# Kernel optimization log

Hardware: AMD Instinct MI355X
Metric: run time of the kernel (lower is better)

Reference implementation:

```python
import jax, jax.numpy as jnp
import numpy as np

FUTURE_K = 16
NEG_BIG = -1e9  # matches masked softmax semantics (invalid slots get exactly 0 weight in fp32)


def setup_inputs() -> dict:
    key = jax.random.key(0)
    hidden_states = jax.random.normal(key, (2, 4096, 1024), dtype=jnp.float32)
    return {"hidden_states": hidden_states}


def reference(hidden_states) -> jnp.ndarray:
    # Windowed future attention: for each position t, attend over the next
    # FUTURE_K hidden states (t+1 .. t+k), masked at the sequence end.
    B, S, H = hidden_states.shape
    k = FUTURE_K
    # pad on the right so every window is full-length
    x_padded = jnp.pad(hidden_states, ((0, 0), (0, k), (0, 0)))  # (B, S+k, H)
    t = jnp.arange(S)
    gidx = t[:, None] + 1 + jnp.arange(k)[None, :]               # (S, k) global indices
    windows = x_padded[:, gidx]                                   # (B, S, k, H)
    valid = gidx < S                                              # (S, k)
    # per-window dot-product scores, masked softmax over window slots
    scores = jnp.einsum('bth,btjh->btj', hidden_states, windows)  # (B, S, k)
    scores = jnp.where(valid[None], scores, NEG_BIG)
    weights = jax.nn.softmax(scores, axis=-1)
    # rows with no valid future (last positions) -> zero summary (torch nan_to_num)
    weights = jnp.where(valid[None], weights, 0.0)
    summary = jnp.einsum('btj,btjh->bth', weights, windows)       # (B, S, H)
    return summary
```

## Files before the change

### kernel.cpp

```cpp
#include <hip/hip_runtime.h>


typedef float f32x4 __attribute__((ext_vector_type(4)));
typedef unsigned int u32;
typedef u32 u32x4 __attribute__((ext_vector_type(4)));
typedef short bf16x8 __attribute__((ext_vector_type(8)));

namespace {
constexpr int kB = 2, kS = 4096, kH = 1024;
constexpr int kWaves = 8;
constexpr int kTilesT = 16;
constexpr int kBlocks = kB * kS / kTilesT;
constexpr int kXCD = 8;
constexpr int kHW = kH / kWaves;
}

__device__ __forceinline__ u32 f32u(float x){ return __builtin_bit_cast(u32, x); }
__device__ __forceinline__ float uf32(u32 x){ return __builtin_bit_cast(float, x); }
__device__ __forceinline__ u32 pkbf(float a, float b){ return (f32u(b)&0xFFFF0000u)|(f32u(a)>>16); }

struct Frag2 { bf16x8 hi, lo; };
__device__ __forceinline__ Frag2 split2(float4 u, float4 v) {
  float fu[8] = {u.x,u.y,u.z,u.w,v.x,v.y,v.z,v.w};
  u32 hw[4], lw[4];
#pragma unroll
  for (int i = 0; i < 4; ++i) {
    float a = fu[2*i], b = fu[2*i+1];
    u32 ua = f32u(a), ub = f32u(b);
    hw[i] = (ub & 0xFFFF0000u) | (ua >> 16);
    float la = a - uf32(ua & 0xFFFF0000u);
    float lb = b - uf32(ub & 0xFFFF0000u);
    lw[i] = (f32u(lb) & 0xFFFF0000u) | (f32u(la) >> 16);
  }
  Frag2 r;
  u32x4 h = {hw[0],hw[1],hw[2],hw[3]}, l = {lw[0],lw[1],lw[2],lw[3]};
  r.hi = __builtin_bit_cast(bf16x8, h);
  r.lo = __builtin_bit_cast(bf16x8, l);
  return r;
}

#define MFMA(A,B,C) __builtin_amdgcn_mfma_f32_16x16x32_bf16((A),(B),(C),0,0,0)

__global__ __launch_bounds__(512, 4)
void fenc_mfma(const float* __restrict__ x, float* __restrict__ out) {
  __shared__ float red[kWaves][2][4][64];
  const int lane = (int)(threadIdx.x & 63), wid = (int)(threadIdx.x >> 6);
  const int g = lane >> 4, c = lane & 15;

  const int vb  = (int)(blockIdx.x % kXCD)*(kBlocks/kXCD) + (int)(blockIdx.x / kXCD);
  const int t0g = vb * kTilesT;
  const int b   = t0g / kS, t0 = t0g % kS;
  const float* __restrict__ xb = x + (size_t)b*kS*kH;
  float* __restrict__ ob = out + (size_t)b*kS*kH;
  const int hw0 = kHW * wid;

  const int ra = (t0 + 1 + c  < kS) ? (t0 + 1 + c)  : (kS - 1);
  const int rb = (t0 + 17 + c < kS) ? (t0 + 17 + c) : (kS - 1);
  const float* qp  = xb + (size_t)(t0 + c)*kH + hw0;
  const float* kpa = xb + (size_t)ra*kH + hw0;
  const float* kpb = xb + (size_t)rb*kH + hw0;

  f32x4 aHH = {0.f,0.f,0.f,0.f}, aHL = aHH, aLH = aHH;
  f32x4 bHH = aHH, bHL = aHH, bLH = aHH;
  __builtin_amdgcn_s_setprio(1);
#pragma unroll
  for (int ks = 0; ks < 4; ++ks) {
    const int off = ks*32 + g*8;
    float4 q0 = *(const float4*)(qp  + off), q1 = *(const float4*)(qp  + off + 4);
    float4 a0 = *(const float4*)(kpa + off), a1 = *(const float4*)(kpa + off + 4);
    float4 b0 = *(const float4*)(kpb + off), b1 = *(const float4*)(kpb + off + 4);
    Frag2 fq = split2(q0, q1), fa = split2(a0, a1), fb = split2(b0, b1);
    aHH = MFMA(fa.hi, fq.hi, aHH);
    aHL = MFMA(fa.hi, fq.lo, aHL);
    aLH = MFMA(fa.lo, fq.hi, aLH);
    bHH = MFMA(fb.hi, fq.hi, bHH);
    bHL = MFMA(fb.hi, fq.lo, bHL);
    bLH = MFMA(fb.lo, fq.hi, bLH);
  }
  __builtin_amdgcn_s_setprio(0);
  f32x4 accA = (aHH + aHL) + aLH;
  f32x4 accB = (bHH + bHL) + bLH;

  const float* vrow[8];
#pragma unroll
  for (int i = 0; i < 8; ++i) {
    const int rv = t0 + 1 + 8*g + i;
    vrow[i] = xb + (size_t)((rv < kS) ? rv : (kS - 1))*kH + hw0 + c;
  }
  float vf[8][8];
#pragma unroll
  for (int nt = 0; nt < 8; ++nt)
#pragma unroll
    for (int i = 0; i < 8; ++i) vf[nt][i] = vrow[i][16*nt];

#pragma unroll
  for (int r = 0; r < 4; ++r) {
    red[wid][0][r][lane] = accA[r];
    red[wid][1][r][lane] = accB[r];
  }
  __syncthreads();
#pragma unroll
  for (int w = 0; w < kWaves; ++w) {
    if (w != wid) {
#pragma unroll
      for (int r = 0; r < 4; ++r) {
        accA[r] += red[w][0][r][lane];
        accB[r] += red[w][1][r][lane];
      }
    }
  }

  float p[2][4];
  float vmax = -1e30f;
#pragma unroll
  for (int T = 0; T < 2; ++T)
#pragma unroll
    for (int r = 0; r < 4; ++r) {
      const int w = 16*T + 4*g + r;
      const bool val = (w >= c) && (w < c + 16) && (t0 + 1 + w < kS);
      const float sv = val ? (T ? accB[r] : accA[r]) : -1e30f;
      p[T][r] = sv;
      vmax = fmaxf(vmax, sv);
    }
  vmax = fmaxf(vmax, __shfl_xor(vmax, 16, 64));
  vmax = fmaxf(vmax, __shfl_xor(vmax, 32, 64));
  float psum = 0.f;
#pragma unroll
  for (int T = 0; T < 2; ++T)
#pragma unroll
    for (int r = 0; r < 4; ++r) {
      const int w = 16*T + 4*g + r;
      const bool val = (w >= c) && (w < c + 16) && (t0 + 1 + w < kS);
      const float e = val ? __expf(p[T][r] - vmax) : 0.f;
      p[T][r] = e;
      psum += e;
    }
  psum += __shfl_xor(psum, 16, 64);
  psum += __shfl_xor(psum, 32, 64);
  const float inv = (psum > 0.f) ? (1.f / psum) : 0.f;
#pragma unroll
  for (int T = 0; T < 2; ++T)
#pragma unroll
    for (int r = 0; r < 4; ++r) p[T][r] *= inv;

  const int se = (g & 1)*32 + c, so = se + 16;
  float slot[8];
#pragma unroll
  for (int r = 0; r < 4; ++r) {
    const float e0 = __shfl(p[0][r], se, 64), e1 = __shfl(p[1][r], se, 64);
    const float o0 = __shfl(p[0][r], so, 64), o1 = __shfl(p[1][r], so, 64);
    slot[r]     = (g >> 1) ? e1 : e0;
    slot[4 + r] = (g >> 1) ? o1 : o0;
  }
  u32x4 pw = { pkbf(slot[0],slot[1]), pkbf(slot[2],slot[3]),
               pkbf(slot[4],slot[5]), pkbf(slot[6],slot[7]) };
  const bf16x8 pa = __builtin_bit_cast(bf16x8, pw);

  f32x4 o[8];
  __builtin_amdgcn_s_setprio(1);
#pragma unroll
  for (int nt = 0; nt < 8; ++nt) {
    u32x4 vw = { pkbf(vf[nt][0],vf[nt][1]), pkbf(vf[nt][2],vf[nt][3]),
                 pkbf(vf[nt][4],vf[nt][5]), pkbf(vf[nt][6],vf[nt][7]) };
    const bf16x8 vfrag = __builtin_bit_cast(bf16x8, vw);
    f32x4 z = {0.f,0.f,0.f,0.f};
    o[nt] = MFMA(pa, vfrag, z);
  }
  __builtin_amdgcn_s_setprio(0);

  float* orow[4];
#pragma unroll
  for (int r = 0; r < 4; ++r)
    orow[r] = ob + (size_t)(t0 + 4*g + r)*kH + hw0 + c;
#pragma unroll
  for (int nt = 0; nt < 8; ++nt)
#pragma unroll
    for (int r = 0; r < 4; ++r)
      orow[r][16*nt] = o[nt][r];
}

extern "C" void kernel_launch(void* const* d_in, const int* in_sizes, int n_in,
                              void* d_out, int out_size, void* d_ws, size_t ws_size,
                              hipStream_t stream) {
  const float* x = (const float*)d_in[0];
  float* out = (float*)d_out;
  hipLaunchKernelGGL(fenc_mfma, dim3(kBlocks), dim3(512), 0, stream, x, out);
}
```

Before: 25.41 us.

## Split hidden dimension of PV output across two blocks per tile

After: 48.81 us. 92.1% more time.

```diff
diff --git a/kernel.cpp b/kernel.cpp
--- a/kernel.cpp
+++ b/kernel.cpp
@@ -10,9 +10,11 @@
 constexpr int kB = 2, kS = 4096, kH = 1024;
 constexpr int kWaves = 8;
 constexpr int kTilesT = 16;
-constexpr int kBlocks = kB * kS / kTilesT;
+constexpr int kHSplit = 2;
+constexpr int kBlocks = kHSplit * kB * kS / kTilesT;
 constexpr int kXCD = 8;
-constexpr int kHW = kH / kWaves;
+constexpr int kHW  = kH / kWaves;
+constexpr int kHPV = kH / kHSplit / kWaves;
 }
 
 __device__ __forceinline__ u32 f32u(float x){ return __builtin_bit_cast(u32, x); }
@@ -41,18 +43,20 @@
 
 #define MFMA(A,B,C) __builtin_amdgcn_mfma_f32_16x16x32_bf16((A),(B),(C),0,0,0)
 
-__global__ __launch_bounds__(512, 4)
+__global__ __launch_bounds__(512, 8)
 void fenc_mfma(const float* __restrict__ x, float* __restrict__ out) {
-  __shared__ float red[kWaves][2][4][64];
+  __shared__ f32x4 red[kWaves][2][64];
   const int lane = (int)(threadIdx.x & 63), wid = (int)(threadIdx.x >> 6);
   const int g = lane >> 4, c = lane & 15;
 
   const int vb  = (int)(blockIdx.x % kXCD)*(kBlocks/kXCD) + (int)(blockIdx.x / kXCD);
-  const int t0g = vb * kTilesT;
+  const int tile = vb >> 1, q = vb & 1;
+  const int t0g = tile * kTilesT;
   const int b   = t0g / kS, t0 = t0g % kS;
   const float* __restrict__ xb = x + (size_t)b*kS*kH;
   float* __restrict__ ob = out + (size_t)b*kS*kH;
-  const int hw0 = kHW * wid;
+  const int hw0  = kHW * wid;
+  const int hpv0 = q * (kH / kHSplit) + kHPV * wid;
 
   const int ra = (t0 + 1 + c  < kS) ? (t0 + 1 + c)  : (kS - 1);
   const int rb = (t0 + 17 + c < kS) ? (t0 + 17 + c) : (kS - 1);
@@ -85,28 +89,19 @@
 #pragma unroll
   for (int i = 0; i < 8; ++i) {
     const int rv = t0 + 1 + 8*g + i;
-    vrow[i] = xb + (size_t)((rv < kS) ? rv : (kS - 1))*kH + hw0 + c;
+    vrow[i] = xb + (size_t)((rv < kS) ? rv : (kS - 1))*kH + hpv0 + c;
   }
-  float vf[8][8];
-#pragma unroll
-  for (int nt = 0; nt < 8; ++nt)
-#pragma unroll
-    for (int i = 0; i < 8; ++i) vf[nt][i] = vrow[i][16*nt];
 
-#pragma unroll
-  for (int r = 0; r < 4; ++r) {
-    red[wid][0][r][lane] = accA[r];
-    red[wid][1][r][lane] = accB[r];
-  }
+  red[wid][0][lane] = accA;
+  red[wid][1][lane] = accB;
   __syncthreads();
 #pragma unroll
   for (int w = 0; w < kWaves; ++w) {
     if (w != wid) {
-#pragma unroll
-      for (int r = 0; r < 4; ++r) {
-        accA[r] += red[w][0][r][lane];
-        accB[r] += red[w][1][r][lane];
-      }
+      const f32x4 pa4 = red[w][0][lane];
+      const f32x4 pb4 = red[w][1][lane];
+      accA += pa4;
+      accB += pb4;
     }
   }
 
@@ -156,12 +151,15 @@
                pkbf(slot[4],slot[5]), pkbf(slot[6],slot[7]) };
   const bf16x8 pa = __builtin_bit_cast(bf16x8, pw);
 
-  f32x4 o[8];
+  f32x4 o[4];
   __builtin_amdgcn_s_setprio(1);
 #pragma unroll
-  for (int nt = 0; nt < 8; ++nt) {
-    u32x4 vw = { pkbf(vf[nt][0],vf[nt][1]), pkbf(vf[nt][2],vf[nt][3]),
-                 pkbf(vf[nt][4],vf[nt][5]), pkbf(vf[nt][6],vf[nt][7]) };
+  for (int nt = 0; nt < 4; ++nt) {
+    float vf[8];
+#pragma unroll
+    for (int i = 0; i < 8; ++i) vf[i] = vrow[i][16*nt];
+    u32x4 vw = { pkbf(vf[0],vf[1]), pkbf(vf[2],vf[3]),
+                 pkbf(vf[4],vf[5]), pkbf(vf[6],vf[7]) };
     const bf16x8 vfrag = __builtin_bit_cast(bf16x8, vw);
     f32x4 z = {0.f,0.f,0.f,0.f};
     o[nt] = MFMA(pa, vfrag, z);
@@ -171,9 +169,9 @@
   float* orow[4];
 #pragma unroll
   for (int r = 0; r < 4; ++r)
-    orow[r] = ob + (size_t)(t0 + 4*g + r)*kH + hw0 + c;
+    orow[r] = ob + (size_t)(t0 + 4*g + r)*kH + hpv0 + c;
 #pragma unroll
-  for (int nt = 0; nt < 8; ++nt)
+  for (int nt = 0; nt < 4; ++nt)
 #pragma unroll
     for (int r = 0; r < 4; ++r)
       orow[r][16*nt] = o[nt][r];
```
